# Performance work log

Hardware: AMD Instinct MI355X
Metric: run time of the kernel (lower is better)

Reference implementation:

```python
import jax, jax.numpy as jnp
import numpy as np

LATENT = 128
HEADS = 4
HEAD_DIM = LATENT // HEADS
NUM_BUCKETS = 32
MAX_DISTANCE = 100000
B, N = 8, 2048


def relative_position_bucket(qpos, kpos):
    """T5-style bidirectional relative position bucketing.
    qpos, kpos: [B, N] int -> buckets [B, N, N] int32 in [0, NUM_BUCKETS).
    """
    rel = kpos[:, None, :] - qpos[:, :, None]  # [B, Nq, Nk]
    half = NUM_BUCKETS // 2
    buckets = (rel > 0).astype(jnp.int32) * half
    arel = jnp.abs(rel)
    max_exact = half // 2
    is_small = arel < max_exact
    # log-spaced buckets for larger distances
    large = max_exact + (
        jnp.log(jnp.maximum(arel, 1).astype(jnp.float32) / max_exact)
        / np.log(MAX_DISTANCE / max_exact)
        * (half - max_exact)
    ).astype(jnp.int32)
    large = jnp.minimum(large, half - 1)
    return buckets + jnp.where(is_small, arel.astype(jnp.int32), large)


def setup_inputs() -> dict:
    key = jax.random.key(0)
    ks = jax.random.split(key, 12)
    s = 0.02
    x = jax.random.normal(ks[0], (B, N, LATENT), dtype=jnp.float32)
    positions = jnp.sort(jax.random.randint(ks[1], (B, N), 0, 1000000), axis=-1)
    mask = jnp.ones((B, N), dtype=bool)
    Wq = jax.random.normal(ks[2], (LATENT, LATENT), dtype=jnp.float32) * s
    bq = jax.random.normal(ks[3], (LATENT,), dtype=jnp.float32) * s
    Wk = jax.random.normal(ks[4], (LATENT, LATENT), dtype=jnp.float32) * s
    bk = jax.random.normal(ks[5], (LATENT,), dtype=jnp.float32) * s
    Wv = jax.random.normal(ks[6], (LATENT, LATENT), dtype=jnp.float32) * s
    bv = jax.random.normal(ks[7], (LATENT,), dtype=jnp.float32) * s
    pos_w = jax.random.normal(ks[8], (NUM_BUCKETS + 1, HEADS), dtype=jnp.float32) * s
    Wo = jax.random.normal(ks[9], (LATENT, LATENT), dtype=jnp.float32) * s
    bo = jax.random.normal(ks[10], (LATENT,), dtype=jnp.float32) * s
    return {"x": x, "positions": positions, "mask": mask,
            "Wq": Wq, "bq": bq, "Wk": Wk, "bk": bk, "Wv": Wv, "bv": bv,
            "pos_w": pos_w, "Wo": Wo, "bo": bo}


def reference(x, positions, mask, Wq, bq, Wk, bk, Wv, bv, pos_w, Wo, bo):
    b, n, _ = x.shape
    # QKV projections, split heads: [b, h, n, d]
    Q = (x @ Wq + bq).reshape(b, n, HEADS, HEAD_DIM).transpose(0, 2, 1, 3)
    K = (x @ Wk + bk).reshape(b, n, HEADS, HEAD_DIM).transpose(0, 2, 1, 3)
    V = (x @ Wv + bv).reshape(b, n, HEADS, HEAD_DIM).transpose(0, 2, 1, 3)
    scores = jnp.einsum("bhqd,bhkd->bhqk", Q, K) / jnp.sqrt(
        jnp.asarray(HEAD_DIM, dtype=x.dtype))
    buckets = relative_position_bucket(positions, positions)  # [b, n, n]
    bias = pos_w[buckets]                  # [b, n, n, h]
    scores = scores + bias.transpose(0, 3, 1, 2)  # [b, h, n, n]
    scores = jnp.where(mask[:, None, None, :], scores, -jnp.inf)
    attn = jax.nn.softmax(scores, axis=-1)
    attn = jnp.nan_to_num(attn, nan=0.0)
    attended = jnp.einsum("bhqk,bhkd->bhqd", attn, V)
    attended = attended.transpose(0, 2, 1, 3).reshape(b, n, LATENT)
    return attended @ Wo + bo
```

## Files before the change

kernel.cpp:

```cpp
#include <hip/hip_runtime.h>
#include <math.h>


#define LOG2E 1.4426950408889634f
#define QKV_SCALE 0.17677669529663687f
#define QS (QKV_SCALE * LOG2E)

typedef _Float16 half8 __attribute__((ext_vector_type(8)));
typedef _Float16 half2v __attribute__((ext_vector_type(2)));
typedef float ffrag __attribute__((ext_vector_type(4)));

#if __has_builtin(__builtin_amdgcn_exp2f)
#define EXP2F __builtin_amdgcn_exp2f
#else
#define EXP2F exp2f
#endif

static __device__ __forceinline__ unsigned short f16bits(float f) {
    return __builtin_bit_cast(unsigned short, (_Float16)f);
}
static __device__ __forceinline__ float h16f(unsigned int bits) {
    return (float)__builtin_bit_cast(_Float16, (unsigned short)(bits & 0xFFFFu));
}
static __device__ __forceinline__ unsigned int pk2(float a, float b) {
    return __builtin_bit_cast(unsigned int, __builtin_amdgcn_cvt_pkrtz(a, b));
}
static __device__ __forceinline__ unsigned int pkmul(unsigned int p, unsigned int w) {
    const half2v r = __builtin_bit_cast(half2v, p) * __builtin_bit_cast(half2v, w);
    return __builtin_bit_cast(unsigned int, r);
}

__device__ __constant__ int SN_TAB[32] = {
    -2000000000,
    -30755, -9458, -2908, -894, -275, -84, -26,
    -7, -6, -5, -4, -3, -2, -1,
    0,
    1, 2, 3, 4, 5, 6, 7,
    8,
    27, 85, 276, 895, 2909, 9459, 30756,
    2000000000 };

__global__ __launch_bounds__(512)
void qkv_seg_kernel(const float* __restrict__ x, const int* __restrict__ positions,
                    const float* __restrict__ Wq, const float* __restrict__ bq,
                    const float* __restrict__ Wk, const float* __restrict__ bk,
                    const float* __restrict__ Wv, const float* __restrict__ bv,
                    const float* __restrict__ Wo,
                    unsigned short* __restrict__ Qb, unsigned short* __restrict__ Kb,
                    unsigned short* __restrict__ Vg2,
                    unsigned int* __restrict__ segtab,
                    unsigned short* __restrict__ Wt_o)
{
    const int tid = threadIdx.x;
    const int wave = tid >> 6, lane = tid & 63;
    const int lq = lane & 15, quad = lane >> 4;
    const int p = blockIdx.x;

    const int token0 = p * 32;
    const int b = token0 >> 11, n0 = token0 & 2047;
    const int colbase = wave * 16;

    half8 xf[2][4];
    #pragma unroll
    for (int m = 0; m < 2; ++m)
        #pragma unroll
        for (int ks = 0; ks < 4; ++ks) {
            const float* xp = x + (size_t)(token0 + m * 16 + lq) * 128 + ks * 32 + quad * 8;
            const float4 a = *(const float4*)xp;
            const float4 c = *(const float4*)(xp + 4);
            xf[m][ks] = __builtin_bit_cast(half8,
                make_int4(pk2(a.x, a.y), pk2(a.z, a.w), pk2(c.x, c.y), pk2(c.z, c.w)));
        }

    #pragma unroll
    for (int which = 0; which < 2; ++which) {
        const float* W  = which ? Wk : Wq;
        const float* bb = which ? bk : bq;
        unsigned short* dst = which ? Kb : Qb;
        const float sc = which ? 1.0f : QS;
        half8 wf[4];
        #pragma unroll
        for (int ks = 0; ks < 4; ++ks) {
            half8 w;
            #pragma unroll
            for (int jj = 0; jj < 8; ++jj) {
                const int k = ks * 32 + quad * 8 + jj;
                w[jj] = (_Float16)(W[k * 128 + colbase + lq] * sc);
            }
            wf[ks] = w;
        }
        const int c0 = colbase + quad * 4;
        float4 bs = *(const float4*)(bb + c0);
        const int h = c0 >> 5, d = c0 & 31;
        #pragma unroll
        for (int m = 0; m < 2; ++m) {
            ffrag acc = {bs.x * sc, bs.y * sc, bs.z * sc, bs.w * sc};
            #pragma unroll
            for (int ks = 0; ks < 4; ++ks)
                acc = __builtin_amdgcn_mfma_f32_16x16x32_f16(wf[ks], xf[m][ks], acc, 0, 0, 0);
            const int n = n0 + m * 16 + lq;
            *(ushort4*)(dst + ((size_t)(b * 4 + h) * 2048 + n) * 32 + d) =
                make_ushort4(f16bits(acc[0]), f16bits(acc[1]),
                             f16bits(acc[2]), f16bits(acc[3]));
        }
    }

    {
        half8 wf[4];
        #pragma unroll
        for (int ks = 0; ks < 4; ++ks) {
            half8 w;
            #pragma unroll
            for (int jj = 0; jj < 8; ++jj) {
                const int k = ks * 32 + quad * 8 + jj;
                w[jj] = (_Float16)Wv[k * 128 + colbase + lq];
            }
            wf[ks] = w;
        }
        const int col = colbase + lq;
        const float bias = bv[col];
        const int h = col >> 5, d = col & 31;
        #pragma unroll
        for (int m = 0; m < 2; ++m) {
            ffrag acc = {bias, bias, bias, bias};
            #pragma unroll
            for (int ks = 0; ks < 4; ++ks)
                acc = __builtin_amdgcn_mfma_f32_16x16x32_f16(xf[m][ks], wf[ks], acc, 0, 0, 0);
            const int nn = n0 + m * 16 + quad * 4;
            const int chunk = nn >> 7, kloc = nn & 127;
            const int win = kloc >> 5, rem = kloc & 31;
            const int hlf = rem >> 4, pg = (rem >> 2) & 3;
            const size_t off = (((size_t)(b * 4 + h) * 16 + chunk) * 512
                                + win * 128 + d * 4 + pg) * 8 + hlf * 4;
            *(ushort4*)(Vg2 + off) = make_ushort4(f16bits(acc[0]), f16bits(acc[1]),
                                                  f16bits(acc[2]), f16bits(acc[3]));
        }
    }

    {
        const int row = p * 32 + (tid >> 4);
        const int bb2 = row >> 11;
        const int* kp = positions + bb2 * 2048;
        const int qp = kp[row & 2047];
        #pragma unroll
        for (int ss = 0; ss < 2; ++ss) {
            const int s = (tid & 15) + ss * 16;
            unsigned int val;
            if (s == 31) {
                val = (2048u << 16) | 31u;
            } else {
                const int bucket = (s < 15) ? (15 - s) : (s == 15 ? 0 : s + 1);
                const int target = qp + SN_TAB[s + 1];
                int lo = 0, hi = 2048;
                while (lo < hi) {
                    const int mid = (lo + hi) >> 1;
                    if (kp[mid] < target) lo = mid + 1; else hi = mid;
                }
                val = ((unsigned)lo << 16) | (unsigned)bucket;
            }
            segtab[row * 32 + s] = val;
        }
    }

    if (tid < 32) {
        const int e = p * 32 + tid;
        const int c = e >> 7, k = e & 127;
        Wt_o[c * 128 + k] = f16bits(Wo[k * 128 + c]);
    }
}

__global__ __launch_bounds__(512, 4)
void attn_kernel(const unsigned short* __restrict__ Qb,
                 const unsigned short* __restrict__ Kb,
                 const unsigned short* __restrict__ Vg2,
                 const unsigned int* __restrict__ segtab,
                 const float* __restrict__ pos_w,
                 unsigned short* __restrict__ att)
{
    __shared__ __align__(16) unsigned int SMEM[4672];
    unsigned int* Sg = SMEM;

    const int tid = threadIdx.x;
    const int wave = __builtin_amdgcn_readfirstlane(tid >> 6);
    const int lane = tid & 63;
    const int lq = lane & 15, quad = lane >> 4;
    const int g = wave >> 2, wg = wave & 3;

    const int qt = blockIdx.x & 15, bh = blockIdx.x >> 4;
    const int b = bh >> 2, h = bh & 3;
    const int q0 = qt * 128;

    const unsigned short* Kg = Kb + (size_t)bh * 65536;
    const unsigned short* Vgb = Vg2 + (size_t)bh * 65536;

    {
        const unsigned int* src = segtab + ((size_t)b * 2048 + q0) * 32;
        #pragma unroll
        for (int it = 0; it < 2; ++it) {
            const int e4 = tid + it * 512;
            uint4 u = *(const uint4*)(src + e4 * 4);
            unsigned int* c = &u.x;
            const int row = e4 >> 3, s0 = (e4 & 7) * 4;
            const int rx = row & 31;
            #pragma unroll
            for (int i2 = 0; i2 < 4; ++i2) {
                const float wfv = __expf(pos_w[(c[i2] & 0xFFFFu) * 4 + h]);
                Sg[row * 32 + ((s0 + i2) ^ rx)] = (c[i2] & 0xFFFF0000u) | f16bits(wfv);
            }
        }
    }
    __syncthreads();

    const int qa = q0 + wg * 32 + lq;
    const int qbn = qa + 16;
    const half8 qfa = *(const half8*)(Qb + ((size_t)bh * 2048 + qa) * 32 + quad * 8);
    const half8 qfb = *(const half8*)(Qb + ((size_t)bh * 2048 + qbn) * 32 + quad * 8);

    half8 ones;
    #pragma unroll
    for (int i = 0; i < 8; ++i) ones[i] = (_Float16)1.0f;

    ffrag o0a = {0.f,0.f,0.f,0.f}, o1a = {0.f,0.f,0.f,0.f}, o2a = {0.f,0.f,0.f,0.f};
    ffrag o0b = {0.f,0.f,0.f,0.f}, o1b = {0.f,0.f,0.f,0.f}, o2b = {0.f,0.f,0.f,0.f};
    int cura = -1, enda = 0; float wfa = 0.f; unsigned int wfa2 = 0;
    int curb = -1, endb = 0; float wfb = 0.f; unsigned int wfb2 = 0;
    const int rowa = wg * 32 + lq, rowb = rowa + 16;
    const int sga = rowa * 32, xa = rowa & 31;
    const int sgb = rowb * 32, xb = rowb & 31;

    half8 kf[2][4], vf[2][4];
    const int gv = (lq * 4 + quad) * 8;

    auto load_k = [&](half8* dst, int idx) {
        const int kb0 = idx * 64;
        #pragma unroll
        for (int j = 0; j < 4; ++j)
            dst[j] = *(const half8*)(Kg + (size_t)(kb0 + j * 16 + lq) * 32 + quad * 8);
    };
    auto load_v = [&](half8* dst, int idx) {
        const unsigned short* vp = Vgb + (size_t)(idx >> 1) * 4096 + (idx & 1) * 2048 + gv;
        dst[0] = *(const half8*)(vp);
        dst[1] = *(const half8*)(vp + 512);
        dst[2] = *(const half8*)(vp + 1024);
        dst[3] = *(const half8*)(vp + 1536);
    };
    auto compute = [&](const half8* karr, const half8* varr, int idx) {
        const int kb0 = idx * 64;
        #pragma unroll
        for (int dw = 0; dw < 2; ++dw) {
            unsigned int pua[4], pub[4];
            #pragma unroll
            for (int T = 0; T < 2; ++T) {
                const half8 kfc = karr[dw * 2 + T];
                ffrag sa = {0.f,0.f,0.f,0.f}, sb = {0.f,0.f,0.f,0.f};
                sa = __builtin_amdgcn_mfma_f32_16x16x32_f16(kfc, qfa, sa, 0, 0, 0);
                sb = __builtin_amdgcn_mfma_f32_16x16x32_f16(kfc, qfb, sb, 0, 0, 0);
                const int kidx = kb0 + dw * 32 + T * 16 + quad * 4;
                if (__builtin_expect(__any(kidx + 3 >= enda), 0)) {
                    float pa[4];
                    #pragma unroll
                    for (int r = 0; r < 4; ++r) {
                        while (kidx + r >= enda) {
                            const unsigned int u = Sg[sga + ((++cura) ^ xa)];
                            enda = (int)(u >> 16); wfa = h16f(u);
                            wfa2 = (u & 0xFFFFu) * 0x10001u;
                        }
                        pa[r] = EXP2F(sa[r]) * wfa;
                    }
                    pua[T * 2 + 0] = pk2(pa[0], pa[1]);
                    pua[T * 2 + 1] = pk2(pa[2], pa[3]);
                } else {
                    pua[T * 2 + 0] = pkmul(pk2(EXP2F(sa[0]), EXP2F(sa[1])), wfa2);
                    pua[T * 2 + 1] = pkmul(pk2(EXP2F(sa[2]), EXP2F(sa[3])), wfa2);
                }
                if (__builtin_expect(__any(kidx + 3 >= endb), 0)) {
                    float pb[4];
                    #pragma unroll
                    for (int r = 0; r < 4; ++r) {
                        while (kidx + r >= endb) {
                            const unsigned int u = Sg[sgb + ((++curb) ^ xb)];
                            endb = (int)(u >> 16); wfb = h16f(u);
                            wfb2 = (u & 0xFFFFu) * 0x10001u;
                        }
                        pb[r] = EXP2F(sb[r]) * wfb;
                    }
                    pub[T * 2 + 0] = pk2(pb[0], pb[1]);
                    pub[T * 2 + 1] = pk2(pb[2], pb[3]);
                } else {
                    pub[T * 2 + 0] = pkmul(pk2(EXP2F(sb[0]), EXP2F(sb[1])), wfb2);
                    pub[T * 2 + 1] = pkmul(pk2(EXP2F(sb[2]), EXP2F(sb[3])), wfb2);
                }
            }
            const half8 A0 = varr[dw * 2];
            const half8 A1 = varr[dw * 2 + 1];
            const half8 Ba = __builtin_bit_cast(half8, make_int4(pua[0], pua[1], pua[2], pua[3]));
            const half8 Bb = __builtin_bit_cast(half8, make_int4(pub[0], pub[1], pub[2], pub[3]));
            o0a = __builtin_amdgcn_mfma_f32_16x16x32_f16(A0, Ba, o0a, 0, 0, 0);
            o1a = __builtin_amdgcn_mfma_f32_16x16x32_f16(A1, Ba, o1a, 0, 0, 0);
            o2a = __builtin_amdgcn_mfma_f32_16x16x32_f16(ones, Ba, o2a, 0, 0, 0);
            o0b = __builtin_amdgcn_mfma_f32_16x16x32_f16(A0, Bb, o0b, 0, 0, 0);
            o1b = __builtin_amdgcn_mfma_f32_16x16x32_f16(A1, Bb, o1b, 0, 0, 0);
            o2b = __builtin_amdgcn_mfma_f32_16x16x32_f16(ones, Bb, o2b, 0, 0, 0);
        }
    };

    load_k(kf[0], g * 2);
    load_v(vf[0], g * 2);

    #pragma unroll 1
    for (int i = 0; i < 8; ++i) {
        const int ci = 2 * i + g;
        load_k(kf[1], ci * 2 + 1);
        load_v(vf[1], ci * 2 + 1);
        compute(kf[0], vf[0], ci * 2);
        if (i < 7) {
            load_k(kf[0], ci * 2 + 4);
            load_v(vf[0], ci * 2 + 4);
        }
        compute(kf[1], vf[1], ci * 2 + 1);
    }

    float lsa = o2a[0], lsb = o2b[0];
    __syncthreads();
    float* scr = (float*)SMEM;
    if (g == 1) {
        float* s = scr + (wg * 64 + lane) * 18;
        #pragma unroll
        for (int j = 0; j < 4; ++j) {
            s[j] = o0a[j]; s[4 + j] = o1a[j]; s[8 + j] = o0b[j]; s[12 + j] = o1b[j];
        }
        s[16] = lsa; s[17] = lsb;
    }
    __syncthreads();
    if (g == 0) {
        const float* s = scr + (wg * 64 + lane) * 18;
        #pragma unroll
        for (int j = 0; j < 4; ++j) {
            o0a[j] += s[j]; o1a[j] += s[4 + j]; o0b[j] += s[8 + j]; o1b[j] += s[12 + j];
        }
        lsa += s[16]; lsb += s[17];
        const float inva = 1.0f / lsa;
        const float invb = 1.0f / lsb;

        unsigned short* da = att + (size_t)(b * 2048 + qa) * 128 + h * 32 + quad * 4;
        uint2 r0, r1;
        r0.x = pk2(o0a[0] * inva, o0a[1] * inva);
        r0.y = pk2(o0a[2] * inva, o0a[3] * inva);
        r1.x = pk2(o1a[0] * inva, o1a[1] * inva);
        r1.y = pk2(o1a[2] * inva, o1a[3] * inva);
        *(uint2*)da = r0;
        *(uint2*)(da + 16) = r1;

        unsigned short* db = att + (size_t)(b * 2048 + qbn) * 128 + h * 32 + quad * 4;
        r0.x = pk2(o0b[0] * invb, o0b[1] * invb);
        r0.y = pk2(o0b[2] * invb, o0b[3] * invb);
        r1.x = pk2(o1b[0] * invb, o1b[1] * invb);
        r1.y = pk2(o1b[2] * invb, o1b[3] * invb);
        *(uint2*)db = r0;
        *(uint2*)(db + 16) = r1;
    }
}

__global__ __launch_bounds__(512)
void out_mfma(const unsigned short* __restrict__ att,
              const unsigned short* __restrict__ Wt_o,
              const float* __restrict__ bo, float* __restrict__ out)
{
    __shared__ __align__(16) unsigned short Xs[64 * 136];
    const int tid = threadIdx.x;
    const int token0 = blockIdx.x * 64;
    #pragma unroll
    for (int it = 0; it < 2; ++it) {
        const int f = tid + it * 512;
        const int row = f >> 4, k0 = (f & 15) << 3;
        const uint4 v = *(const uint4*)(att + (size_t)(token0 + row) * 128 + k0);
        *(uint4*)(Xs + row * 136 + k0) = v;
    }
    __syncthreads();

    const int wave = tid >> 6, lane = tid & 63;
    const int lq = lane & 15, quad = lane >> 4;
    const int colbase = wave * 16;

    half8 wf[4];
    #pragma unroll
    for (int ks = 0; ks < 4; ++ks)
        wf[ks] = *(const half8*)(Wt_o + (colbase + lq) * 128 + ks * 32 + quad * 8);
    const float4 bv = *(const float4*)(bo + colbase + quad * 4);

    #pragma unroll
    for (int msub = 0; msub < 4; ++msub) {
        ffrag acc = {bv.x, bv.y, bv.z, bv.w};
        #pragma unroll
        for (int ks = 0; ks < 4; ++ks) {
            const half8 xf = *(const half8*)(Xs + (msub * 16 + lq) * 136 + ks * 32 + quad * 8);
            acc = __builtin_amdgcn_mfma_f32_16x16x32_f16(wf[ks], xf, acc, 0, 0, 0);
        }
        const int c0 = colbase + quad * 4;
        *(float4*)(out + (size_t)(token0 + msub * 16 + lq) * 128 + c0) =
            make_float4(acc[0], acc[1], acc[2], acc[3]);
    }
}

extern "C" void kernel_launch(void* const* d_in, const int* in_sizes, int n_in,
                              void* d_out, int out_size, void* d_ws, size_t ws_size,
                              hipStream_t stream)
{
    const float* x         = (const float*)d_in[0];
    const int*   positions = (const int*)d_in[1];
    const float* Wq = (const float*)d_in[3];
    const float* bq = (const float*)d_in[4];
    const float* Wk = (const float*)d_in[5];
    const float* bk = (const float*)d_in[6];
    const float* Wv = (const float*)d_in[7];
    const float* bv = (const float*)d_in[8];
    const float* pw = (const float*)d_in[9];
    const float* Wo = (const float*)d_in[10];
    const float* bo = (const float*)d_in[11];
    float* out = (float*)d_out;

    unsigned short* Qb  = (unsigned short*)d_ws;
    unsigned short* Kb  = Qb + 2097152;
    unsigned short* Vg2 = Kb + 2097152;
    unsigned short* att = Vg2 + 2097152;
    unsigned int* segtab = (unsigned int*)(att + 2097152);
    unsigned short* Wt_o = (unsigned short*)(segtab + 524288);

    qkv_seg_kernel<<<512, 512, 0, stream>>>(x, positions, Wq, bq, Wk, bk, Wv, bv,
                                            Wo, Qb, Kb, Vg2, segtab, Wt_o);
    attn_kernel<<<512, 512, 0, stream>>>(Qb, Kb, Vg2, segtab, pw, att);
    out_mfma<<<256, 512, 0, stream>>>(att, Wt_o, bo, out);
}
```

Baseline: 172.0 us.

## Drop split-K reduction in attention; one 16-query tile per wave, 1024 blocks

The attention kernel now uses 256-thread blocks that each cover 64 queries, launched as 1024 blocks. Each wave owns 16 queries and walks all 2048 keys alone with a two-stage register double buffer of 32 keys. This removes the old split of the key range across two wave groups, along with its shared-memory reduction and extra barriers. In exchange, each wave reuses every K/V fragment for only 16 queries instead of 32, which doubles K/V global loads per query, and the serial key loop is twice as long.

New measurement: 171.4 us. Within noise of the previous version (-0.3%).

```diff
diff --git a/kernel.cpp b/kernel.cpp
--- a/kernel.cpp
+++ b/kernel.cpp
@@ -169,7 +169,7 @@
     }
 }
 
-__global__ __launch_bounds__(512, 4)
+__global__ __launch_bounds__(256, 4)
 void attn_kernel(const unsigned short* __restrict__ Qb,
                  const unsigned short* __restrict__ Kb,
                  const unsigned short* __restrict__ Vg2,
@@ -177,18 +177,16 @@
                  const float* __restrict__ pos_w,
                  unsigned short* __restrict__ att)
 {
-    __shared__ __align__(16) unsigned int SMEM[4672];
-    unsigned int* Sg = SMEM;
+    __shared__ unsigned int Sg[64 * 32];
 
     const int tid = threadIdx.x;
     const int wave = __builtin_amdgcn_readfirstlane(tid >> 6);
     const int lane = tid & 63;
     const int lq = lane & 15, quad = lane >> 4;
-    const int g = wave >> 2, wg = wave & 3;
-
-    const int qt = blockIdx.x & 15, bh = blockIdx.x >> 4;
+
+    const int qt = blockIdx.x & 31, bh = blockIdx.x >> 5;
     const int b = bh >> 2, h = bh & 3;
-    const int q0 = qt * 128;
+    const int q0 = qt * 64;
 
     const unsigned short* Kg = Kb + (size_t)bh * 65536;
     const unsigned short* Vgb = Vg2 + (size_t)bh * 65536;
@@ -197,7 +195,7 @@
         const unsigned int* src = segtab + ((size_t)b * 2048 + q0) * 32;
         #pragma unroll
         for (int it = 0; it < 2; ++it) {
-            const int e4 = tid + it * 512;
+            const int e4 = tid + it * 256;
             uint4 u = *(const uint4*)(src + e4 * 4);
             unsigned int* c = &u.x;
             const int row = e4 >> 3, s0 = (e4 & 7) * 4;
@@ -211,154 +209,78 @@
     }
     __syncthreads();
 
-    const int qa = q0 + wg * 32 + lq;
-    const int qbn = qa + 16;
-    const half8 qfa = *(const half8*)(Qb + ((size_t)bh * 2048 + qa) * 32 + quad * 8);
-    const half8 qfb = *(const half8*)(Qb + ((size_t)bh * 2048 + qbn) * 32 + quad * 8);
+    const int qg = q0 + wave * 16 + lq;
+    const half8 qf = *(const half8*)(Qb + ((size_t)bh * 2048 + qg) * 32 + quad * 8);
 
     half8 ones;
     #pragma unroll
     for (int i = 0; i < 8; ++i) ones[i] = (_Float16)1.0f;
 
-    ffrag o0a = {0.f,0.f,0.f,0.f}, o1a = {0.f,0.f,0.f,0.f}, o2a = {0.f,0.f,0.f,0.f};
-    ffrag o0b = {0.f,0.f,0.f,0.f}, o1b = {0.f,0.f,0.f,0.f}, o2b = {0.f,0.f,0.f,0.f};
-    int cura = -1, enda = 0; float wfa = 0.f; unsigned int wfa2 = 0;
-    int curb = -1, endb = 0; float wfb = 0.f; unsigned int wfb2 = 0;
-    const int rowa = wg * 32 + lq, rowb = rowa + 16;
-    const int sga = rowa * 32, xa = rowa & 31;
-    const int sgb = rowb * 32, xb = rowb & 31;
-
-    half8 kf[2][4], vf[2][4];
+    ffrag o0 = {0.f,0.f,0.f,0.f}, o1 = {0.f,0.f,0.f,0.f}, o2 = {0.f,0.f,0.f,0.f};
+    int cur = -1, endk = 0; float wfs = 0.f; unsigned int wf2 = 0;
+    const int row = wave * 16 + lq;
+    const int sg0 = row * 32, xr = row & 31;
+
+    half8 kf2[2][2], vf2[2][2];
     const int gv = (lq * 4 + quad) * 8;
 
-    auto load_k = [&](half8* dst, int idx) {
-        const int kb0 = idx * 64;
-        #pragma unroll
-        for (int j = 0; j < 4; ++j)
-            dst[j] = *(const half8*)(Kg + (size_t)(kb0 + j * 16 + lq) * 32 + quad * 8);
+    auto load_stage = [&](int buf, int s) {
+        kf2[buf][0] = *(const half8*)(Kg + (size_t)(s * 32 + lq) * 32 + quad * 8);
+        kf2[buf][1] = *(const half8*)(Kg + (size_t)(s * 32 + 16 + lq) * 32 + quad * 8);
+        const unsigned short* vp = Vgb + (size_t)s * 1024 + gv;
+        vf2[buf][0] = *(const half8*)(vp);
+        vf2[buf][1] = *(const half8*)(vp + 512);
     };
-    auto load_v = [&](half8* dst, int idx) {
-        const unsigned short* vp = Vgb + (size_t)(idx >> 1) * 4096 + (idx & 1) * 2048 + gv;
-        dst[0] = *(const half8*)(vp);
-        dst[1] = *(const half8*)(vp + 512);
-        dst[2] = *(const half8*)(vp + 1024);
-        dst[3] = *(const half8*)(vp + 1536);
+    auto compute_stage = [&](int buf, int s) {
+        unsigned int pu[4];
+        #pragma unroll
+        for (int T = 0; T < 2; ++T) {
+            ffrag sa = {0.f,0.f,0.f,0.f};
+            sa = __builtin_amdgcn_mfma_f32_16x16x32_f16(kf2[buf][T], qf, sa, 0, 0, 0);
+            const int kidx = s * 32 + T * 16 + quad * 4;
+            if (__builtin_expect(__any(kidx + 3 >= endk), 0)) {
+                float pa[4];
+                #pragma unroll
+                for (int r = 0; r < 4; ++r) {
+                    while (kidx + r >= endk) {
+                        const unsigned int u = Sg[sg0 + ((++cur) ^ xr)];
+                        endk = (int)(u >> 16); wfs = h16f(u);
+                        wf2 = (u & 0xFFFFu) * 0x10001u;
+                    }
+                    pa[r] = EXP2F(sa[r]) * wfs;
+                }
+                pu[T * 2 + 0] = pk2(pa[0], pa[1]);
+                pu[T * 2 + 1] = pk2(pa[2], pa[3]);
+            } else {
+                pu[T * 2 + 0] = pkmul(pk2(EXP2F(sa[0]), EXP2F(sa[1])), wf2);
+                pu[T * 2 + 1] = pkmul(pk2(EXP2F(sa[2]), EXP2F(sa[3])), wf2);
+            }
+        }
+        const half8 Ba = __builtin_bit_cast(half8, make_int4(pu[0], pu[1], pu[2], pu[3]));
+        o0 = __builtin_amdgcn_mfma_f32_16x16x32_f16(vf2[buf][0], Ba, o0, 0, 0, 0);
+        o1 = __builtin_amdgcn_mfma_f32_16x16x32_f16(vf2[buf][1], Ba, o1, 0, 0, 0);
+        o2 = __builtin_amdgcn_mfma_f32_16x16x32_f16(ones, Ba, o2, 0, 0, 0);
     };
-    auto compute = [&](const half8* karr, const half8* varr, int idx) {
-        const int kb0 = idx * 64;
-        #pragma unroll
-        for (int dw = 0; dw < 2; ++dw) {
-            unsigned int pua[4], pub[4];
-            #pragma unroll
-            for (int T = 0; T < 2; ++T) {
-                const half8 kfc = karr[dw * 2 + T];
-                ffrag sa = {0.f,0.f,0.f,0.f}, sb = {0.f,0.f,0.f,0.f};
-                sa = __builtin_amdgcn_mfma_f32_16x16x32_f16(kfc, qfa, sa, 0, 0, 0);
-                sb = __builtin_amdgcn_mfma_f32_16x16x32_f16(kfc, qfb, sb, 0, 0, 0);
-                const int kidx = kb0 + dw * 32 + T * 16 + quad * 4;
-                if (__builtin_expect(__any(kidx + 3 >= enda), 0)) {
-                    float pa[4];
-                    #pragma unroll
-                    for (int r = 0; r < 4; ++r) {
-                        while (kidx + r >= enda) {
-                            const unsigned int u = Sg[sga + ((++cura) ^ xa)];
-                            enda = (int)(u >> 16); wfa = h16f(u);
-                            wfa2 = (u & 0xFFFFu) * 0x10001u;
-                        }
-                        pa[r] = EXP2F(sa[r]) * wfa;
-                    }
-                    pua[T * 2 + 0] = pk2(pa[0], pa[1]);
-                    pua[T * 2 + 1] = pk2(pa[2], pa[3]);
-                } else {
-                    pua[T * 2 + 0] = pkmul(pk2(EXP2F(sa[0]), EXP2F(sa[1])), wfa2);
-                    pua[T * 2 + 1] = pkmul(pk2(EXP2F(sa[2]), EXP2F(sa[3])), wfa2);
-                }
-                if (__builtin_expect(__any(kidx + 3 >= endb), 0)) {
-                    float pb[4];
-                    #pragma unroll
-                    for (int r = 0; r < 4; ++r) {
-                        while (kidx + r >= endb) {
-                            const unsigned int u = Sg[sgb + ((++curb) ^ xb)];
-                            endb = (int)(u >> 16); wfb = h16f(u);
-                            wfb2 = (u & 0xFFFFu) * 0x10001u;
-                        }
-                        pb[r] = EXP2F(sb[r]) * wfb;
-                    }
-                    pub[T * 2 + 0] = pk2(pb[0], pb[1]);
-                    pub[T * 2 + 1] = pk2(pb[2], pb[3]);
-                } else {
-                    pub[T * 2 + 0] = pkmul(pk2(EXP2F(sb[0]), EXP2F(sb[1])), wfb2);
-                    pub[T * 2 + 1] = pkmul(pk2(EXP2F(sb[2]), EXP2F(sb[3])), wfb2);
-                }
-            }
-            const half8 A0 = varr[dw * 2];
-            const half8 A1 = varr[dw * 2 + 1];
-            const half8 Ba = __builtin_bit_cast(half8, make_int4(pua[0], pua[1], pua[2], pua[3]));
-            const half8 Bb = __builtin_bit_cast(half8, make_int4(pub[0], pub[1], pub[2], pub[3]));
-            o0a = __builtin_amdgcn_mfma_f32_16x16x32_f16(A0, Ba, o0a, 0, 0, 0);
-            o1a = __builtin_amdgcn_mfma_f32_16x16x32_f16(A1, Ba, o1a, 0, 0, 0);
-            o2a = __builtin_amdgcn_mfma_f32_16x16x32_f16(ones, Ba, o2a, 0, 0, 0);
-            o0b = __builtin_amdgcn_mfma_f32_16x16x32_f16(A0, Bb, o0b, 0, 0, 0);
-            o1b = __builtin_amdgcn_mfma_f32_16x16x32_f16(A1, Bb, o1b, 0, 0, 0);
-            o2b = __builtin_amdgcn_mfma_f32_16x16x32_f16(ones, Bb, o2b, 0, 0, 0);
-        }
-    };
-
-    load_k(kf[0], g * 2);
-    load_v(vf[0], g * 2);
-
+
+    load_stage(0, 0);
     #pragma unroll 1
-    for (int i = 0; i < 8; ++i) {
-        const int ci = 2 * i + g;
-        load_k(kf[1], ci * 2 + 1);
-        load_v(vf[1], ci * 2 + 1);
-        compute(kf[0], vf[0], ci * 2);
-        if (i < 7) {
-            load_k(kf[0], ci * 2 + 4);
-            load_v(vf[0], ci * 2 + 4);
-        }
-        compute(kf[1], vf[1], ci * 2 + 1);
-    }
-
-    float lsa = o2a[0], lsb = o2b[0];
-    __syncthreads();
-    float* scr = (float*)SMEM;
-    if (g == 1) {
-        float* s = scr + (wg * 64 + lane) * 18;
-        #pragma unroll
-        for (int j = 0; j < 4; ++j) {
-            s[j] = o0a[j]; s[4 + j] = o1a[j]; s[8 + j] = o0b[j]; s[12 + j] = o1b[j];
-        }
-        s[16] = lsa; s[17] = lsb;
-    }
-    __syncthreads();
-    if (g == 0) {
-        const float* s = scr + (wg * 64 + lane) * 18;
-        #pragma unroll
-        for (int j = 0; j < 4; ++j) {
-            o0a[j] += s[j]; o1a[j] += s[4 + j]; o0b[j] += s[8 + j]; o1b[j] += s[12 + j];
-        }
-        lsa += s[16]; lsb += s[17];
-        const float inva = 1.0f / lsa;
-        const float invb = 1.0f / lsb;
-
-        unsigned short* da = att + (size_t)(b * 2048 + qa) * 128 + h * 32 + quad * 4;
-        uint2 r0, r1;
-        r0.x = pk2(o0a[0] * inva, o0a[1] * inva);
-        r0.y = pk2(o0a[2] * inva, o0a[3] * inva);
-        r1.x = pk2(o1a[0] * inva, o1a[1] * inva);
-        r1.y = pk2(o1a[2] * inva, o1a[3] * inva);
-        *(uint2*)da = r0;
-        *(uint2*)(da + 16) = r1;
-
-        unsigned short* db = att + (size_t)(b * 2048 + qbn) * 128 + h * 32 + quad * 4;
-        r0.x = pk2(o0b[0] * invb, o0b[1] * invb);
-        r0.y = pk2(o0b[2] * invb, o0b[3] * invb);
-        r1.x = pk2(o1b[0] * invb, o1b[1] * invb);
-        r1.y = pk2(o1b[2] * invb, o1b[3] * invb);
-        *(uint2*)db = r0;
-        *(uint2*)(db + 16) = r1;
-    }
+    for (int s = 0; s < 32; ++s) {
+        const int s0 = 2 * s;
+        load_stage(1, s0 + 1);
+        compute_stage(0, s0);
+        if (s < 31) load_stage(0, s0 + 2);
+        compute_stage(1, s0 + 1);
+    }
+
+    const float inv = 1.0f / o2[0];
+    unsigned short* dst = att + (size_t)(b * 2048 + qg) * 128 + h * 32 + quad * 4;
+    uint2 r0, r1;
+    r0.x = pk2(o0[0] * inv, o0[1] * inv);
+    r0.y = pk2(o0[2] * inv, o0[3] * inv);
+    r1.x = pk2(o1[0] * inv, o1[1] * inv);
+    r1.y = pk2(o1[2] * inv, o1[3] * inv);
+    *(uint2*)dst = r0;
+    *(uint2*)(dst + 16) = r1;
 }
 
 __global__ __launch_bounds__(512)
@@ -428,6 +350,6 @@
 
     qkv_seg_kernel<<<512, 512, 0, stream>>>(x, positions, Wq, bq, Wk, bk, Wv, bv,
                                             Wo, Qb, Kb, Vg2, segtab, Wt_o);
-    attn_kernel<<<512, 512, 0, stream>>>(Qb, Kb, Vg2, segtab, pw, att);
+    attn_kernel<<<1024, 256, 0, stream>>>(Qb, Kb, Vg2, segtab, pw, att);
     out_mfma<<<256, 512, 0, stream>>>(att, Wt_o, bo, out);
 }
```
